# Performance work log

Measured on AMD Instinct MI355X. Metric: run time of the kernel, lower is better.

## Reference

```python
import jax, jax.numpy as jnp
import numpy as np

EMBED = 1024  # point_net_embedding_dim
H1, H2 = 512, 256  # head_hidden_layer_sizes


def _init(key, shape, fan_in):
    return jax.random.normal(key, shape, dtype=jnp.float32) / jnp.sqrt(jnp.float32(fan_in))


def setup_inputs() -> dict:
    key = jax.random.key(0)
    ks = jax.random.split(key, 13)
    B, N = 256, 1024
    x = jax.random.normal(ks[0], (B, N, 3), dtype=jnp.float32)
    # PointNet shared per-point MLP: 3 -> 64 -> 128 -> EMBED (ReLU), max-pool over points
    W1 = _init(ks[1], (3, 64), 3);        b1 = jnp.zeros((64,), jnp.float32)
    W2 = _init(ks[2], (64, 128), 64);     b2 = jnp.zeros((128,), jnp.float32)
    W3 = _init(ks[3], (128, EMBED), 128); b3 = jnp.zeros((EMBED,), jnp.float32)
    # Head MLP: EMBED -> 512 -> 256 -> 9 (no final activation)
    Wh1 = _init(ks[4], (EMBED, H1), EMBED); bh1 = jnp.zeros((H1,), jnp.float32)
    Wh2 = _init(ks[5], (H1, H2), H1);       bh2 = jnp.zeros((H2,), jnp.float32)
    Wh3 = _init(ks[6], (H2, 9), H2);        bh3 = jnp.zeros((9,), jnp.float32)
    return {"x": x, "W1": W1, "b1": b1, "W2": W2, "b2": b2, "W3": W3, "b3": b3,
            "Wh1": Wh1, "bh1": bh1, "Wh2": Wh2, "bh2": bh2, "Wh3": Wh3, "bh3": bh3}


def svd_projection(M):
    # Project raw 3x3 matrices onto SO(3): R = U diag(1,1,det(U V^T)) V^T
    U, S, Vh = jnp.linalg.svd(M, full_matrices=False)
    det = jnp.linalg.det(jnp.einsum('...ij,...jk->...ik', U, Vh))
    d = jnp.stack([jnp.ones_like(det), jnp.ones_like(det), det], axis=-1)  # [..., 3]
    return jnp.einsum('...ij,...j,...jk->...ik', U, d, Vh)


def reference(x, W1, b1, W2, b2, W3, b3, Wh1, bh1, Wh2, bh2, Wh3, bh3):
    # Shared per-point MLP (ReLU), final_activation=ReLU, then max-pool over points
    h = jax.nn.relu(x @ W1 + b1)          # [B, N, 64]
    h = jax.nn.relu(h @ W2 + b2)          # [B, N, 128]
    h = jax.nn.relu(h @ W3 + b3)          # [B, N, EMBED]
    g = jnp.max(h, axis=-2)               # [B, EMBED] global feature
    # Head MLP -> raw 3x3
    z = jax.nn.relu(g @ Wh1 + bh1)
    z = jax.nn.relu(z @ Wh2 + bh2)
    raw = (z @ Wh3 + bh3).reshape(*x.shape[:-2], 3, 3)
    return svd_projection(raw)
```

## Files before the change

### kernel.cpp

```cpp
#include <hip/hip_runtime.h>
#include <math.h>

typedef _Float16 f16;
typedef _Float16 f16x8 __attribute__((ext_vector_type(8)));
typedef float f32x4 __attribute__((ext_vector_type(4)));

__device__ __forceinline__ void glds16(const void* g, void* l) {
    __builtin_amdgcn_global_load_lds(
        (const __attribute__((address_space(1))) unsigned int*)g,
        (__attribute__((address_space(3))) unsigned int*)l, 16, 0, 0);
}

__global__ __launch_bounds__(256) void prep_wt(
    const float* __restrict__ w3, const float* __restrict__ w2,
    f16* __restrict__ w3t, f16* __restrict__ w2t)
{
    __shared__ float t[64][65];
    int bid = blockIdx.x;
    int tid = threadIdx.x;
    if (bid < 32) {
        int kt = bid & 1, nt = bid >> 1;
        int k0 = kt*64, n0 = nt*64;
#pragma unroll
        for (int j = 0; j < 16; j++) {
            int r = j*4 + (tid >> 6), c = tid & 63;
            t[r][c] = w3[(size_t)(k0+r)*1024 + n0 + c];
        }
        __syncthreads();
#pragma unroll
        for (int j = 0; j < 16; j++) {
            int n = j*4 + (tid >> 6), k = tid & 63;
            w3t[(size_t)(n0+n)*128 + k0 + k] = (f16)t[k][n];
        }
    } else {
        int n0 = (bid - 32) * 64;
#pragma unroll
        for (int j = 0; j < 16; j++) {
            int r = j*4 + (tid >> 6), c = tid & 63;
            t[r][c] = w2[(size_t)r*128 + n0 + c];
        }
        __syncthreads();
#pragma unroll
        for (int j = 0; j < 16; j++) {
            int n = j*4 + (tid >> 6), k = tid & 63;
            w2t[(size_t)(n0+n)*64 + k] = (f16)t[k][n];
        }
    }
}

__global__ __launch_bounds__(256, 2) void pointnet_l12(
    const float* __restrict__ x,
    const float* __restrict__ W1, const float* __restrict__ b1,
    const f16* __restrict__ w2t, const float* __restrict__ b2,
    f16* __restrict__ h2)
{
    __shared__ float xs[512*3];
    __shared__ float w1s[192], b1s[64], b2s[128];
    __shared__ __align__(16) f16 h2s[128*136];

    int tid = threadIdx.x;
    int P0 = blockIdx.x * 512;
    for (int i = tid; i < 1536; i += 256) xs[i] = x[(size_t)P0*3 + i];
    if (tid < 192) w1s[tid] = W1[tid];
    else b1s[tid - 192] = b1[tid - 192];
    if (tid < 128) b2s[tid] = b2[tid];

    int lane = tid & 63, wid = tid >> 6;
    int wr = wid & 1, wc = wid >> 1;
    int lrow = lane & 15, quad = lane >> 4;

    f16x8 bf[4][2];
#pragma unroll
    for (int ct = 0; ct < 4; ct++)
#pragma unroll
        for (int kc = 0; kc < 2; kc++)
            bf[ct][kc] = *(const f16x8*)(w2t + (size_t)(wc*64 + ct*16 + lrow)*64 + kc*32 + quad*8);

    __syncthreads();

    for (int mt = 0; mt < 4; mt++) {
        f32x4 acc[4][4];
#pragma unroll
        for (int rt = 0; rt < 4; rt++)
#pragma unroll
            for (int ct = 0; ct < 4; ct++)
                acc[rt][ct] = (f32x4){0.f, 0.f, 0.f, 0.f};

#pragma unroll
        for (int kc = 0; kc < 2; kc++) {
            float wa[8], wb[8], wcv[8], bv[8];
#pragma unroll
            for (int j = 0; j < 8; j++) {
                int k = kc*32 + quad*8 + j;
                wa[j] = w1s[k]; wb[j] = w1s[64+k]; wcv[j] = w1s[128+k]; bv[j] = b1s[k];
            }
            f16x8 af[4];
#pragma unroll
            for (int rt = 0; rt < 4; rt++) {
                int p = mt*128 + wr*64 + rt*16 + lrow;
                float x0 = xs[p*3], x1 = xs[p*3+1], x2 = xs[p*3+2];
#pragma unroll
                for (int j = 0; j < 8; j++) {
                    float v = fmaf(x2, wcv[j], fmaf(x1, wb[j], fmaf(x0, wa[j], bv[j])));
                    af[rt][j] = (f16)fmaxf(v, 0.f);
                }
            }
#pragma unroll
            for (int rt = 0; rt < 4; rt++)
#pragma unroll
                for (int ct = 0; ct < 4; ct++)
                    acc[rt][ct] = __builtin_amdgcn_mfma_f32_16x16x32_f16(af[rt], bf[ct][kc], acc[rt][ct], 0, 0, 0);
        }

        __syncthreads();
#pragma unroll
        for (int rt = 0; rt < 4; rt++)
#pragma unroll
            for (int ct = 0; ct < 4; ct++) {
                int col  = wc*64 + ct*16 + lrow;
                float bb = b2s[col];
                int rowb = wr*64 + rt*16 + quad*4;
#pragma unroll
                for (int r = 0; r < 4; r++) {
                    float v = fmaxf(acc[rt][ct][r] + bb, 0.f);
                    h2s[(rowb + r)*136 + col] = (f16)v;
                }
            }
        __syncthreads();
        size_t gbase = ((size_t)P0 + (size_t)mt*128) * 128;
#pragma unroll
        for (int i = 0; i < 8; i++) {
            int e = i*256 + tid;
            int row = e >> 4, c = e & 15;
            f16x8 v = *(const f16x8*)(h2s + row*136 + c*8);
            *(f16x8*)(h2 + gbase + (size_t)row*128 + ((c ^ (row & 15)) * 8)) = v;
        }
    }
}

__global__ __launch_bounds__(256, 2) void pointnet_l3_max(
    const f16* __restrict__ h2,
    const f16* __restrict__ w3t,
    const float* __restrict__ b3,
    float* __restrict__ g)
{
    __shared__ __align__(16) f16 atile[128 * 128];

    int i  = blockIdx.x;
    int b  = i & 255, nb = i >> 8;
    int tid = threadIdx.x;
    int lane = tid & 63, wid = tid >> 6;
    int lrow = lane & 15, quad = lane >> 4;
    int col0 = nb*256 + wid*64;

    f16x8 bf[4][4];
#pragma unroll
    for (int ct = 0; ct < 4; ct++)
#pragma unroll
        for (int kc = 0; kc < 4; kc++)
            bf[ct][kc] = *(const f16x8*)(w3t + (size_t)(col0 + ct*16 + lrow)*128 + kc*32 + quad*8);

    float cmax[4] = {-3.0e38f, -3.0e38f, -3.0e38f, -3.0e38f};
    const f16* abase = h2 + (size_t)b * 1024 * 128;

    for (int m0 = 0; m0 < 1024; m0 += 128) {
        __syncthreads();
        {
            const f16* gsrc = abase + (size_t)m0 * 128;
#pragma unroll
            for (int s = 0; s < 8; s++) {
                int chunk = wid*512 + s*64 + lane;
                glds16(gsrc + chunk*8, atile + (wid*512 + s*64)*8);
            }
        }
        __syncthreads();

#pragma unroll
        for (int half = 0; half < 2; half++) {
            f32x4 acc[4][4];
#pragma unroll
            for (int rt = 0; rt < 4; rt++)
#pragma unroll
                for (int ct = 0; ct < 4; ct++)
                    acc[rt][ct] = (f32x4){0.f, 0.f, 0.f, 0.f};
#pragma unroll
            for (int kc = 0; kc < 4; kc++) {
                f16x8 af[4];
#pragma unroll
                for (int rt = 0; rt < 4; rt++) {
                    int row  = half*64 + rt*16 + lrow;
                    int slot = (kc*4 + quad) ^ lrow;
                    af[rt] = *(const f16x8*)(atile + row*128 + slot*8);
                }
#pragma unroll
                for (int rt = 0; rt < 4; rt++)
#pragma unroll
                    for (int ct = 0; ct < 4; ct++)
                        acc[rt][ct] = __builtin_amdgcn_mfma_f32_16x16x32_f16(af[rt], bf[ct][kc], acc[rt][ct], 0, 0, 0);
            }
#pragma unroll
            for (int rt = 0; rt < 4; rt++)
#pragma unroll
                for (int ct = 0; ct < 4; ct++)
#pragma unroll
                    for (int r = 0; r < 4; r++)
                        cmax[ct] = fmaxf(cmax[ct], acc[rt][ct][r]);
        }
    }

#pragma unroll
    for (int ct = 0; ct < 4; ct++) {
        cmax[ct] = fmaxf(cmax[ct], __shfl_xor(cmax[ct], 16, 64));
        cmax[ct] = fmaxf(cmax[ct], __shfl_xor(cmax[ct], 32, 64));
    }
    if (quad == 0) {
#pragma unroll
        for (int ct = 0; ct < 4; ct++) {
            int cg = col0 + ct*16 + lrow;
            g[(size_t)b*1024 + cg] = fmaxf(cmax[ct] + b3[cg], 0.f);
        }
    }
}

__global__ __launch_bounds__(256) void head_l1(
    const float* __restrict__ g, const float* __restrict__ Wh1,
    float* __restrict__ zp1)
{
    __shared__ float gs4[4][256];
    int cb = blockIdx.x, bb = blockIdx.y, kc = blockIdx.z;
    int tid = threadIdx.x;
    int b0 = bb * 4;
    int kbase = kc * 256;
#pragma unroll
    for (int j = 0; j < 4; j++) {
        int i = tid + j*256;
        gs4[i >> 8][i & 255] = g[(size_t)(b0 + (i >> 8))*1024 + kbase + (i & 255)];
    }
    __syncthreads();

    int c = cb*256 + tid;
    float acc[4] = {0.f, 0.f, 0.f, 0.f};
#pragma unroll 1
    for (int k = 0; k < 256; k += 8) {
        float w[8];
#pragma unroll
        for (int j = 0; j < 8; j++) w[j] = Wh1[(size_t)(kbase+k+j)*512 + c];
#pragma unroll
        for (int r = 0; r < 4; r++) {
            float4 a = *(const float4*)&gs4[r][k];
            float4 bq = *(const float4*)&gs4[r][k+4];
            acc[r] = fmaf(a.x, w[0], acc[r]);
            acc[r] = fmaf(a.y, w[1], acc[r]);
            acc[r] = fmaf(a.z, w[2], acc[r]);
            acc[r] = fmaf(a.w, w[3], acc[r]);
            acc[r] = fmaf(bq.x, w[4], acc[r]);
            acc[r] = fmaf(bq.y, w[5], acc[r]);
            acc[r] = fmaf(bq.z, w[6], acc[r]);
            acc[r] = fmaf(bq.w, w[7], acc[r]);
        }
    }
#pragma unroll
    for (int r = 0; r < 4; r++)
        zp1[((size_t)kc*256 + b0 + r)*512 + c] = acc[r];
}

__global__ __launch_bounds__(256) void head_l2(
    const float* __restrict__ zp1, const float* __restrict__ bh1,
    const float* __restrict__ Wh2, float* __restrict__ zp2)
{
    __shared__ float z1s[2][128];
    int bb = blockIdx.x, kc2 = blockIdx.y;
    int tid = threadIdx.x;
    int b0 = bb * 2;
    int kb = kc2 * 128;
    {
        int row = tid >> 7, kk = tid & 127;
        int col = kb + kk;
        float v = bh1[col];
#pragma unroll
        for (int j = 0; j < 4; j++)
            v += zp1[((size_t)j*256 + b0 + row)*512 + col];
        z1s[row][kk] = fmaxf(v, 0.f);
    }
    __syncthreads();

    int c = tid;
    float acc0 = 0.f, acc1 = 0.f;
#pragma unroll 1
    for (int k = 0; k < 128; k += 8) {
        float w[8];
#pragma unroll
        for (int j = 0; j < 8; j++) w[j] = Wh2[(size_t)(kb+k+j)*256 + c];
        float4 a0 = *(const float4*)&z1s[0][k];
        float4 a1 = *(const float4*)&z1s[0][k+4];
        float4 d0 = *(const float4*)&z1s[1][k];
        float4 d1 = *(const float4*)&z1s[1][k+4];
        acc0 = fmaf(a0.x, w[0], acc0);  acc1 = fmaf(d0.x, w[0], acc1);
        acc0 = fmaf(a0.y, w[1], acc0);  acc1 = fmaf(d0.y, w[1], acc1);
        acc0 = fmaf(a0.z, w[2], acc0);  acc1 = fmaf(d0.z, w[2], acc1);
        acc0 = fmaf(a0.w, w[3], acc0);  acc1 = fmaf(d0.w, w[3], acc1);
        acc0 = fmaf(a1.x, w[4], acc0);  acc1 = fmaf(d1.x, w[4], acc1);
        acc0 = fmaf(a1.y, w[5], acc0);  acc1 = fmaf(d1.y, w[5], acc1);
        acc0 = fmaf(a1.z, w[6], acc0);  acc1 = fmaf(d1.z, w[6], acc1);
        acc0 = fmaf(a1.w, w[7], acc0);  acc1 = fmaf(d1.w, w[7], acc1);
    }
    zp2[((size_t)kc2*256 + b0    )*256 + c] = acc0;
    zp2[((size_t)kc2*256 + b0 + 1)*256 + c] = acc1;
}

__device__ inline void jrot(double S[3][3], double V[3][3], int p, int q)
{
    double apq = S[p][q];
    if (fabs(apq) < 1e-36) return;
    double tau = (S[q][q] - S[p][p]) / (2.0 * apq);
    double t = (tau >= 0.0 ? 1.0 : -1.0) / (fabs(tau) + sqrt(1.0 + tau*tau));
    double c = 1.0 / sqrt(1.0 + t*t);
    double s = t * c;
    for (int k = 0; k < 3; k++) {
        double skp = S[k][p], skq = S[k][q];
        S[k][p] = c*skp - s*skq;  S[k][q] = s*skp + c*skq;
    }
    for (int k = 0; k < 3; k++) {
        double spk = S[p][k], sqk = S[q][k];
        S[p][k] = c*spk - s*sqk;  S[q][k] = s*spk + c*sqk;
    }
    for (int k = 0; k < 3; k++) {
        double vkp = V[k][p], vkq = V[k][q];
        V[k][p] = c*vkp - s*vkq;  V[k][q] = s*vkp + c*vkq;
    }
}

__device__ void svd_so3(const float* Mf, float* Rout)
{
    double M[3][3], S[3][3], V[3][3];
    for (int i = 0; i < 3; i++)
        for (int j = 0; j < 3; j++) M[i][j] = (double)Mf[3*i+j];
    for (int i = 0; i < 3; i++)
        for (int j = 0; j < 3; j++)
            S[i][j] = M[0][i]*M[0][j] + M[1][i]*M[1][j] + M[2][i]*M[2][j];
    for (int i = 0; i < 3; i++)
        for (int j = 0; j < 3; j++) V[i][j] = (i == j) ? 1.0 : 0.0;
    for (int it = 0; it < 10; it++) {
        jrot(S, V, 0, 1); jrot(S, V, 0, 2); jrot(S, V, 1, 2);
    }
    double lam[3] = {S[0][0], S[1][1], S[2][2]};
    int i0 = 0, i1 = 1, i2 = 2, tt;
    if (lam[i0] < lam[i1]) { tt = i0; i0 = i1; i1 = tt; }
    if (lam[i0] < lam[i2]) { tt = i0; i0 = i2; i2 = tt; }
    if (lam[i1] < lam[i2]) { tt = i1; i1 = i2; i2 = tt; }
    double v0[3], v1[3], v2[3];
    for (int k = 0; k < 3; k++) { v0[k] = V[k][i0]; v1[k] = V[k][i1]; v2[k] = V[k][i2]; }
    double u1[3], u2[3], u3[3];
    for (int i = 0; i < 3; i++) u1[i] = M[i][0]*v0[0] + M[i][1]*v0[1] + M[i][2]*v0[2];
    double n1 = sqrt(u1[0]*u1[0] + u1[1]*u1[1] + u1[2]*u1[2]) + 1e-300;
    for (int i = 0; i < 3; i++) u1[i] /= n1;
    for (int i = 0; i < 3; i++) u2[i] = M[i][0]*v1[0] + M[i][1]*v1[1] + M[i][2]*v1[2];
    double d12 = u1[0]*u2[0] + u1[1]*u2[1] + u1[2]*u2[2];
    for (int i = 0; i < 3; i++) u2[i] -= d12*u1[i];
    double n2 = sqrt(u2[0]*u2[0] + u2[1]*u2[1] + u2[2]*u2[2]) + 1e-300;
    for (int i = 0; i < 3; i++) u2[i] /= n2;
    u3[0] = u1[1]*u2[2] - u1[2]*u2[1];
    u3[1] = u1[2]*u2[0] - u1[0]*u2[2];
    u3[2] = u1[0]*u2[1] - u1[1]*u2[0];
    double c12x = v1[1]*v2[2] - v1[2]*v2[1];
    double c12y = v1[2]*v2[0] - v1[0]*v2[2];
    double c12z = v1[0]*v2[1] - v1[1]*v2[0];
    double detV = v0[0]*c12x + v0[1]*c12y + v0[2]*c12z;
    for (int i = 0; i < 3; i++)
        for (int j = 0; j < 3; j++)
            Rout[3*i+j] = (float)(u1[i]*v0[j] + u2[i]*v1[j] + detV*u3[i]*v2[j]);
}

__global__ __launch_bounds__(128) void head_l3_svd(
    const float* __restrict__ zp2, const float* __restrict__ bh2,
    const float* __restrict__ Wh3, const float* __restrict__ bh3,
    float* __restrict__ out)
{
    __shared__ float z2s[8][256];
    __shared__ float wh3s[2304];
    __shared__ float raws[8][12];
    int b0 = blockIdx.x * 8;
    int tid = threadIdx.x;

    for (int i = tid; i < 2304; i += 128) wh3s[i] = Wh3[i];
    for (int i = tid; i < 8*256; i += 128) {
        int row = i >> 8, kk = i & 255;
        float v = bh2[kk];
#pragma unroll
        for (int j = 0; j < 4; j++)
            v += zp2[((size_t)j*256 + b0 + row)*256 + kk];
        z2s[row][kk] = fmaxf(v, 0.f);
    }
    __syncthreads();

    if (tid < 72) {
        int r = tid / 9, c = tid % 9;
        float acc = bh3[c];
#pragma unroll 8
        for (int k = 0; k < 256; k++) acc = fmaf(z2s[r][k], wh3s[k*9 + c], acc);
        raws[r][c] = acc;
    }
    __syncthreads();

    if (tid < 8) svd_so3(&raws[tid][0], out + (size_t)(b0 + tid)*9);
}

extern "C" void kernel_launch(void* const* d_in, const int* in_sizes, int n_in,
                              void* d_out, int out_size, void* d_ws, size_t ws_size,
                              hipStream_t stream)
{
    const float* x   = (const float*)d_in[0];
    const float* W1  = (const float*)d_in[1];
    const float* b1  = (const float*)d_in[2];
    const float* W2  = (const float*)d_in[3];
    const float* b2  = (const float*)d_in[4];
    const float* W3  = (const float*)d_in[5];
    const float* b3  = (const float*)d_in[6];
    const float* Wh1 = (const float*)d_in[7];
    const float* bh1 = (const float*)d_in[8];
    const float* Wh2 = (const float*)d_in[9];
    const float* bh2 = (const float*)d_in[10];
    const float* Wh3 = (const float*)d_in[11];
    const float* bh3 = (const float*)d_in[12];
    float* out = (float*)d_out;

    char* ws = (char*)d_ws;
    f16*   h2  = (f16*)ws;
    f16*   w3t = (f16*)(ws + (size_t)67108864);
    f16*   w2t = (f16*)(ws + (size_t)67108864 + 262144);
    float* g   = (float*)(ws + (size_t)67108864 + 262144 + 16384);
    float* zp1 = (float*)(ws + (size_t)67108864 + 262144 + 16384 + 1048576);
    float* zp2 = (float*)(ws + (size_t)67108864 + 262144 + 16384 + 1048576 + 2097152);

    prep_wt<<<34, 256, 0, stream>>>(W3, W2, w3t, w2t);
    pointnet_l12<<<512, 256, 0, stream>>>(x, W1, b1, w2t, b2, h2);
    pointnet_l3_max<<<1024, 256, 0, stream>>>(h2, w3t, b3, g);
    dim3 gridH1(2, 64, 4);
    head_l1<<<gridH1, 256, 0, stream>>>(g, Wh1, zp1);
    dim3 gridH2(128, 4);
    head_l2<<<gridH2, 256, 0, stream>>>(zp1, bh1, Wh2, zp2);
    head_l3_svd<<<32, 128, 0, stream>>>(zp2, bh2, Wh3, bh3, out);
}
```

Before: 191.5 us.

## Drop weight prep kernel and double-buffer activation tiles in layer-3 max kernel

Removes the separate transpose/convert kernel for W2 and W3, instead having each block gather and convert the fp32 weights into f16 MFMA fragments directly. The layer-3 max kernel now double-buffers its LDS activation tile so the next tile's global-to-LDS load overlaps MFMA work on the current one, removing one barrier per iteration. This trades a launch and a round-trip for strided, repeated weight reads across 1024 blocks and doubles LDS usage, which could limit occupancy.

New measurement: 189.4 us. About the same (-1.1%).

```diff
diff --git a/kernel.cpp b/kernel.cpp
--- a/kernel.cpp
+++ b/kernel.cpp
@@ -11,47 +11,10 @@
         (__attribute__((address_space(3))) unsigned int*)l, 16, 0, 0);
 }
 
-__global__ __launch_bounds__(256) void prep_wt(
-    const float* __restrict__ w3, const float* __restrict__ w2,
-    f16* __restrict__ w3t, f16* __restrict__ w2t)
-{
-    __shared__ float t[64][65];
-    int bid = blockIdx.x;
-    int tid = threadIdx.x;
-    if (bid < 32) {
-        int kt = bid & 1, nt = bid >> 1;
-        int k0 = kt*64, n0 = nt*64;
-#pragma unroll
-        for (int j = 0; j < 16; j++) {
-            int r = j*4 + (tid >> 6), c = tid & 63;
-            t[r][c] = w3[(size_t)(k0+r)*1024 + n0 + c];
-        }
-        __syncthreads();
-#pragma unroll
-        for (int j = 0; j < 16; j++) {
-            int n = j*4 + (tid >> 6), k = tid & 63;
-            w3t[(size_t)(n0+n)*128 + k0 + k] = (f16)t[k][n];
-        }
-    } else {
-        int n0 = (bid - 32) * 64;
-#pragma unroll
-        for (int j = 0; j < 16; j++) {
-            int r = j*4 + (tid >> 6), c = tid & 63;
-            t[r][c] = w2[(size_t)r*128 + n0 + c];
-        }
-        __syncthreads();
-#pragma unroll
-        for (int j = 0; j < 16; j++) {
-            int n = j*4 + (tid >> 6), k = tid & 63;
-            w2t[(size_t)(n0+n)*64 + k] = (f16)t[k][n];
-        }
-    }
-}
-
 __global__ __launch_bounds__(256, 2) void pointnet_l12(
     const float* __restrict__ x,
     const float* __restrict__ W1, const float* __restrict__ b1,
-    const f16* __restrict__ w2t, const float* __restrict__ b2,
+    const float* __restrict__ W2, const float* __restrict__ b2,
     f16* __restrict__ h2)
 {
     __shared__ float xs[512*3];
@@ -73,8 +36,12 @@
 #pragma unroll
     for (int ct = 0; ct < 4; ct++)
 #pragma unroll
-        for (int kc = 0; kc < 2; kc++)
-            bf[ct][kc] = *(const f16x8*)(w2t + (size_t)(wc*64 + ct*16 + lrow)*64 + kc*32 + quad*8);
+        for (int kc = 0; kc < 2; kc++) {
+            int col = wc*64 + ct*16 + lrow;
+#pragma unroll
+            for (int j = 0; j < 8; j++)
+                bf[ct][kc][j] = (f16)W2[(size_t)(kc*32 + quad*8 + j)*128 + col];
+        }
 
     __syncthreads();
 
@@ -140,11 +107,11 @@
 
 __global__ __launch_bounds__(256, 2) void pointnet_l3_max(
     const f16* __restrict__ h2,
-    const f16* __restrict__ w3t,
+    const float* __restrict__ W3,
     const float* __restrict__ b3,
     float* __restrict__ g)
 {
-    __shared__ __align__(16) f16 atile[128 * 128];
+    __shared__ __align__(16) f16 atile[2][128 * 128];
 
     int i  = blockIdx.x;
     int b  = i & 255, nb = i >> 8;
@@ -157,24 +124,35 @@
 #pragma unroll
     for (int ct = 0; ct < 4; ct++)
 #pragma unroll
-        for (int kc = 0; kc < 4; kc++)
-            bf[ct][kc] = *(const f16x8*)(w3t + (size_t)(col0 + ct*16 + lrow)*128 + kc*32 + quad*8);
+        for (int kc = 0; kc < 4; kc++) {
+            int col = col0 + ct*16 + lrow;
+#pragma unroll
+            for (int j = 0; j < 8; j++)
+                bf[ct][kc][j] = (f16)W3[(size_t)(kc*32 + quad*8 + j)*1024 + col];
+        }
 
     float cmax[4] = {-3.0e38f, -3.0e38f, -3.0e38f, -3.0e38f};
     const f16* abase = h2 + (size_t)b * 1024 * 128;
 
+    {
+        const f16* gsrc = abase;
+#pragma unroll
+        for (int s = 0; s < 8; s++)
+            glds16(gsrc + (wid*512 + s*64 + lane)*8, atile[0] + (wid*512 + s*64)*8);
+    }
+
+    int cur = 0;
     for (int m0 = 0; m0 < 1024; m0 += 128) {
         __syncthreads();
-        {
-            const f16* gsrc = abase + (size_t)m0 * 128;
-#pragma unroll
-            for (int s = 0; s < 8; s++) {
-                int chunk = wid*512 + s*64 + lane;
-                glds16(gsrc + chunk*8, atile + (wid*512 + s*64)*8);
-            }
-        }
-        __syncthreads();
-
+        if (m0 + 128 < 1024) {
+            const f16* gsrc = abase + (size_t)(m0 + 128) * 128;
+            f16* ldst = atile[cur ^ 1];
+#pragma unroll
+            for (int s = 0; s < 8; s++)
+                glds16(gsrc + (wid*512 + s*64 + lane)*8, ldst + (wid*512 + s*64)*8);
+        }
+
+        const f16* at = atile[cur];
 #pragma unroll
         for (int half = 0; half < 2; half++) {
             f32x4 acc[4][4];
@@ -190,7 +168,7 @@
                 for (int rt = 0; rt < 4; rt++) {
                     int row  = half*64 + rt*16 + lrow;
                     int slot = (kc*4 + quad) ^ lrow;
-                    af[rt] = *(const f16x8*)(atile + row*128 + slot*8);
+                    af[rt] = *(const f16x8*)(at + row*128 + slot*8);
                 }
 #pragma unroll
                 for (int rt = 0; rt < 4; rt++)
@@ -206,6 +184,7 @@
                     for (int r = 0; r < 4; r++)
                         cmax[ct] = fmaxf(cmax[ct], acc[rt][ct][r]);
         }
+        cur ^= 1;
     }
 
 #pragma unroll
@@ -426,15 +405,12 @@
 
     char* ws = (char*)d_ws;
     f16*   h2  = (f16*)ws;
-    f16*   w3t = (f16*)(ws + (size_t)67108864);
-    f16*   w2t = (f16*)(ws + (size_t)67108864 + 262144);
-    float* g   = (float*)(ws + (size_t)67108864 + 262144 + 16384);
-    float* zp1 = (float*)(ws + (size_t)67108864 + 262144 + 16384 + 1048576);
-    float* zp2 = (float*)(ws + (size_t)67108864 + 262144 + 16384 + 1048576 + 2097152);
-
-    prep_wt<<<34, 256, 0, stream>>>(W3, W2, w3t, w2t);
-    pointnet_l12<<<512, 256, 0, stream>>>(x, W1, b1, w2t, b2, h2);
-    pointnet_l3_max<<<1024, 256, 0, stream>>>(h2, w3t, b3, g);
+    float* g   = (float*)(ws + (size_t)67108864);
+    float* zp1 = (float*)(ws + (size_t)67108864 + 1048576);
+    float* zp2 = (float*)(ws + (size_t)67108864 + 1048576 + 2097152);
+
+    pointnet_l12<<<512, 256, 0, stream>>>(x, W1, b1, W2, b2, h2);
+    pointnet_l3_max<<<1024, 256, 0, stream>>>(h2, W3, b3, g);
     dim3 gridH1(2, 64, 4);
     head_l1<<<gridH1, 256, 0, stream>>>(g, Wh1, zp1);
     dim3 gridH2(128, 4);
```
